# Kernel tuning notes

Hardware: AMD Instinct MI355X
Metric: run time of the kernel (lower is better)

## Reference

```python
import jax, jax.numpy as jnp
import numpy as np
import math

BS, S, D = 1, 2048, 1024
H = 16
DK = D // H  # 64


def _log_sparse_neighbor_mask(seq_len):
    """mask[i,j]=True iff j==i, or j in [i-k, i) with k=seq_len//2, or i-j is a power of 2.
    Matches generate_log_sparse_plus_neighbors_mask(seq_len, seq_len//2)."""
    k = seq_len // 2
    i = jnp.arange(seq_len, dtype=jnp.int32)[:, None]
    j = jnp.arange(seq_len, dtype=jnp.int32)[None, :]
    diff = i - j
    neighbor = (diff >= 0) & (diff <= k)  # includes diagonal (diff==0)
    pow2 = (diff > 0) & ((diff & (diff - 1)) == 0)
    return neighbor | pow2  # [seq_len, seq_len] bool


def setup_inputs() -> dict:
    key = jax.random.key(0)
    ks = jax.random.split(key, 9)
    std = 0.02
    return {
        "Q": jax.random.normal(ks[0], (BS, S, D), dtype=jnp.float32),
        "Wq": jax.random.normal(ks[1], (D, H * DK), dtype=jnp.float32) * std,
        "bq": jnp.zeros((H * DK,), dtype=jnp.float32),
        "Wk": jax.random.normal(ks[2], (D, H * DK), dtype=jnp.float32) * std,
        "bk": jnp.zeros((H * DK,), dtype=jnp.float32),
        "Wv": jax.random.normal(ks[3], (D, H * DK), dtype=jnp.float32) * std,
        "bv": jnp.zeros((H * DK,), dtype=jnp.float32),
        "Wo": jax.random.normal(ks[4], (H * DK, D), dtype=jnp.float32) * std,
        "bo": jnp.zeros((D,), dtype=jnp.float32),
    }


def reference(Q, Wq, bq, Wk, bk, Wv, bv, Wo, bo):
    bs, s, d = Q.shape
    # QKV projections -> [bs, h, s, dk]
    q = (Q @ Wq + bq).reshape(bs, s, H, DK).transpose(0, 2, 1, 3)
    k = (Q @ Wk + bk).reshape(bs, s, H, DK).transpose(0, 2, 1, 3)
    v = (Q @ Wv + bv).reshape(bs, s, H, DK).transpose(0, 2, 1, 3)

    # log_sparse_attention: scale is 1/sqrt(d_k); mask regenerated internally
    mask = _log_sparse_neighbor_mask(s)  # [s, s] bool
    scores = jnp.einsum("bhqd,bhkd->bhqk", q, k) / math.sqrt(DK)
    scores = jnp.where(mask[None, None, :, :], scores, -jnp.inf)
    attn = jax.nn.softmax(scores, axis=-1)  # [bs, h, s, s]
    out = jnp.einsum("bhqk,bhkd->bhqd", attn, v)

    # merge heads + output projection
    out = out.transpose(0, 2, 1, 3).reshape(bs, s, H * DK)
    out = out @ Wo + bo
    return (out, attn)
```

## Files before the change

### kernel.cpp

```cpp
#include <hip/hip_runtime.h>

#define SEQ 2048
#define DM 1024
#define NH 16
#define DKH 64
#define BAND 1024
#define QKV 3072
#define QBLK 32
#define PBW 1064

typedef __attribute__((ext_vector_type(8))) __bf16 bf16x8;
typedef __attribute__((ext_vector_type(4))) __bf16 bf16x4;
typedef __attribute__((ext_vector_type(4))) float f32x4;

static __device__ __forceinline__ f32x4 mfma16(bf16x8 a, bf16x8 b, f32x4 c) {
  return __builtin_amdgcn_mfma_f32_16x16x32_bf16(a, b, c, 0, 0, 0);
}

#define GLOAD16(gp, lp)                                                        \
  __builtin_amdgcn_global_load_lds(                                            \
      (const __attribute__((address_space(1))) void*)(gp),                     \
      (__attribute__((address_space(3))) void*)(lp), 16, 0, 0)

struct PrepArgs {
  const float* win[4];
  __bf16* wout[4];
  const float* Q;
  __bf16* Qb;
};
__global__ void prep(PrepArgs P) {
  int z = blockIdx.z;
  if (z < 4) {
    __shared__ float t[32][33];
    const float* in = P.win[z];
    __bf16* out = P.wout[z];
    int c0 = blockIdx.x * 32, r0 = blockIdx.y * 32;
    int tx = threadIdx.x, ty = threadIdx.y;
    for (int r = ty; r < 32; r += 8)
      t[r][tx] = in[(size_t)(r0 + r) * DM + c0 + tx];
    __syncthreads();
    for (int r = ty; r < 32; r += 8)
      out[(size_t)(c0 + r) * DM + r0 + tx] = (__bf16)t[tx][r];
  } else {
    int t = threadIdx.y * 32 + threadIdx.x;
    int base = (blockIdx.y * 32 + blockIdx.x) * 512 + t;
#pragma unroll
    for (int u = 0; u < 2; u++) {
      int i = base + u * 256;
      float4 v = reinterpret_cast<const float4*>(P.Q)[i];
      bf16x4 o = {(__bf16)v.x, (__bf16)v.y, (__bf16)v.z, (__bf16)v.w};
      reinterpret_cast<bf16x4*>(P.Qb)[i] = o;
    }
  }
}

template <int BM, int BN, bool BF16OUT, bool VOUT>
__global__ __launch_bounds__(256) void gemm_lds(
    const __bf16* __restrict__ A, const __bf16* __restrict__ BT,
    const float* __restrict__ b0, const float* __restrict__ b1,
    const float* __restrict__ b2, float* __restrict__ Cf,
    __bf16* __restrict__ Cb, __bf16* __restrict__ VT, int M, int N, int K) {
  constexpr int BK = 64;
  constexpr int FM = BM / 32;
  constexpr int FN = BN / 32;
  constexpr int LA = BM * BK * 2 / (256 * 16);
  constexpr int LB = BN * BK * 2 / (256 * 16);
  __shared__ __bf16 lA[2][BM * BK];
  __shared__ __bf16 lB[2][BN * BK];
  int tid = threadIdx.x;
  int lane = tid & 63;
  int l15 = lane & 15, lg = lane >> 4;
  int w = tid >> 6;
  int nwg = gridDim.x * gridDim.y;
  int bid = blockIdx.y * gridDim.x + blockIdx.x;
  int swz = (bid & 7) * (nwg >> 3) + (bid >> 3);
  int bx = swz % gridDim.x;
  int by = swz / gridDim.x;
  int row0 = by * BM;
  int col0 = bx * BN;
  int sec = col0 >> 10;
  const float* bias = sec == 0 ? b0 : (sec == 1 ? b1 : b2);
  int cbase = col0 & (DM - 1);
  int wr = (w >> 1) * (BM / 2);
  int wc = (w & 1) * (BN / 2);
  f32x4 acc[FM][FN] = {};

  auto stage = [&](int b, int kt) {
#pragma unroll
    for (int s = 0; s < LA; s++) {
      int u = tid + s * 256;
      int r = u >> 3;
      int cc = (u & 7) ^ (r & 7);
      GLOAD16(A + (size_t)(row0 + r) * K + kt * BK + cc * 8,
              (char*)lA[b] + u * 16);
    }
#pragma unroll
    for (int s = 0; s < LB; s++) {
      int u = tid + s * 256;
      int r = u >> 3;
      int cc = (u & 7) ^ (r & 7);
      GLOAD16(BT + (size_t)(col0 + r) * K + kt * BK + cc * 8,
              (char*)lB[b] + u * 16);
    }
  };

  const int T = K / BK;
  stage(0, 0);
  stage(1, 1);
  for (int t = 0; t < T; t++) {
    if (t + 1 < T)
      asm volatile("s_waitcnt vmcnt(%0)" ::"i"(LA + LB) : "memory");
    else
      asm volatile("s_waitcnt vmcnt(0)" ::: "memory");
    __builtin_amdgcn_s_barrier();
    int cur = t & 1;
    bf16x8 af[2][FM], bfr[2][FN];
#pragma unroll
    for (int kh = 0; kh < 2; kh++) {
#pragma unroll
      for (int mi = 0; mi < FM; mi++) {
        int r = wr + mi * 16 + l15;
        af[kh][mi] = *(const bf16x8*)((const char*)lA[cur] + r * 128 +
                                      ((((kh << 2) | lg) ^ (r & 7)) << 4));
      }
#pragma unroll
      for (int ni = 0; ni < FN; ni++) {
        int r = wc + ni * 16 + l15;
        bfr[kh][ni] = *(const bf16x8*)((const char*)lB[cur] + r * 128 +
                                       ((((kh << 2) | lg) ^ (r & 7)) << 4));
      }
    }
    __builtin_amdgcn_s_setprio(1);
#pragma unroll
    for (int kh = 0; kh < 2; kh++)
#pragma unroll
      for (int mi = 0; mi < FM; mi++)
#pragma unroll
        for (int ni = 0; ni < FN; ni++)
          acc[mi][ni] = mfma16(af[kh][mi], bfr[kh][ni], acc[mi][ni]);
    __builtin_amdgcn_s_setprio(0);
    __builtin_amdgcn_s_barrier();
    if (t + 2 < T) stage(cur, t + 2);
  }

  if (VOUT && sec == 2) {
#pragma unroll
    for (int mi = 0; mi < FM; mi++) {
      int row = row0 + wr + mi * 16 + lg * 4;
#pragma unroll
      for (int ni = 0; ni < FN; ni++) {
        int hd = cbase + wc + ni * 16 + l15;
        float b = bias[hd];
        bf16x4 pk;
#pragma unroll
        for (int r = 0; r < 4; r++) pk[r] = (__bf16)(acc[mi][ni][r] + b);
        *(bf16x4*)&VT[(size_t)hd * SEQ + row] = pk;
      }
    }
    return;
  }
#pragma unroll
  for (int mi = 0; mi < FM; mi++) {
    int row = row0 + wr + mi * 16 + lg * 4;
#pragma unroll
    for (int ni = 0; ni < FN; ni++) {
      int col = col0 + wc + ni * 16 + l15;
      float b = bias[(cbase + wc + ni * 16 + l15) & (DM - 1)];
#pragma unroll
      for (int r = 0; r < 4; r++) {
        float v = acc[mi][ni][r] + b;
        if constexpr (BF16OUT)
          Cb[(size_t)(row + r) * N + col] = (__bf16)v;
        else
          Cf[(size_t)(row + r) * N + col] = v;
      }
    }
  }
}

__global__ __launch_bounds__(256, 2) void attn_fused(
    const __bf16* __restrict__ qkvb, const __bf16* __restrict__ VT,
    float* __restrict__ attn_out, __bf16* __restrict__ pvb) {
  __shared__ __bf16 pbuf[QBLK][PBW];
  __shared__ float wsum[4][QBLK];
  __shared__ float sinv[QBLK];

  int nwg = gridDim.x * gridDim.y;
  int bid = blockIdx.y * gridDim.x + blockIdx.x;
  int swz = (bid & 7) * (nwg >> 3) + (bid >> 3);
  int h = swz / (SEQ / QBLK);
  int i0 = (swz % (SEQ / QBLK)) * QBLK;

  int tid = threadIdx.x, lane = tid & 63, w = tid >> 6;
  int l15 = lane & 15, lg = lane >> 4;

  int jlo = i0 - BAND;
  if (jlo < 0) jlo = 0;
  int ntiles = (i0 + QBLK - jlo) >> 4;
  int n = ntiles * 16;

  const __bf16* qptr0 = qkvb + (size_t)(i0 + l15) * QKV + h * DKH + lg * 8;
  const __bf16* qptr1 = qptr0 + (size_t)16 * QKV;
  bf16x8 aq0 = *(const bf16x8*)qptr0;
  bf16x8 aq1 = *(const bf16x8*)(qptr0 + 32);
  bf16x8 aq2 = *(const bf16x8*)qptr1;
  bf16x8 aq3 = *(const bf16x8*)(qptr1 + 32);
  const __bf16* kbase = qkvb + DM + h * DKH + lg * 8;

  float sm0[4] = {0.f, 0.f, 0.f, 0.f};
  float sm1[4] = {0.f, 0.f, 0.f, 0.f};
  for (int t = w; t < ntiles; t += 4) {
    int jb = jlo + t * 16;
    const __bf16* kptr = kbase + (size_t)(jb + l15) * QKV;
    bf16x8 k0 = *(const bf16x8*)kptr;
    bf16x8 k1 = *(const bf16x8*)(kptr + 32);
    f32x4 acc0 = {0.f, 0.f, 0.f, 0.f};
    f32x4 acc1 = {0.f, 0.f, 0.f, 0.f};
    __builtin_amdgcn_s_setprio(1);
    acc0 = mfma16(aq0, k0, acc0);
    acc0 = mfma16(aq1, k1, acc0);
    acc1 = mfma16(aq2, k0, acc1);
    acc1 = mfma16(aq3, k1, acc1);
    __builtin_amdgcn_s_setprio(0);
    int col = jb + l15;
    int x = jb - jlo + l15;
#pragma unroll
    for (int r = 0; r < 4; r++) {
      int i = i0 + lg * 4 + r;
      float e0 = 0.f;
      if (col <= i && i - col <= BAND) {
        e0 = __expf(acc0[r] * 0.125f);
        sm0[r] += e0;
      }
      pbuf[lg * 4 + r][x] = (__bf16)e0;
      int i2 = i + 16;
      float e1 = 0.f;
      if (col <= i2 && i2 - col <= BAND) {
        e1 = __expf(acc1[r] * 0.125f);
        sm1[r] += e1;
      }
      pbuf[16 + lg * 4 + r][x] = (__bf16)e1;
    }
  }
#pragma unroll
  for (int o = 1; o < 16; o <<= 1)
#pragma unroll
    for (int r = 0; r < 4; r++) {
      sm0[r] += __shfl_xor(sm0[r], o);
      sm1[r] += __shfl_xor(sm1[r], o);
    }
  if (l15 == 0)
#pragma unroll
    for (int r = 0; r < 4; r++) {
      wsum[w][lg * 4 + r] = sm0[r];
      wsum[w][16 + lg * 4 + r] = sm1[r];
    }
  __syncthreads();
  if (tid < QBLK)
    sinv[tid] = 1.f / (wsum[0][tid] + wsum[1][tid] + wsum[2][tid] + wsum[3][tid]);
  __syncthreads();

  f32x4* abase = (f32x4*)(attn_out + ((size_t)h * SEQ + i0) * SEQ);
  for (int idx = tid; idx < QBLK * (SEQ / 4); idx += 256) {
    int row = idx >> 9;
    int j4 = idx & 511;
    int x = j4 * 4 - jlo;
    bool valid = (unsigned)x < (unsigned)n;
    int xc = valid ? x : 0;
    bf16x4 v4 = *(const bf16x4*)&pbuf[row][xc];
    float inv = valid ? sinv[row] : 0.f;
    f32x4 o = {(float)v4[0] * inv, (float)v4[1] * inv, (float)v4[2] * inv,
               (float)v4[3] * inv};
    __builtin_nontemporal_store(o, abase + idx);
  }

  f32x4 acc0 = {0.f, 0.f, 0.f, 0.f};
  f32x4 acc1 = {0.f, 0.f, 0.f, 0.f};
  int d0 = w * 16;
  const __bf16* vtp = VT + ((size_t)h * DKH + d0 + l15) * SEQ;
  for (int kt = 0; kt < ntiles; kt += 2) {
    int kk = kt * 16;
    bf16x8 pa0 = *(const bf16x8*)&pbuf[l15][kk + lg * 8];
    bf16x8 pa1 = *(const bf16x8*)&pbuf[16 + l15][kk + lg * 8];
    bf16x8 vf = *(const bf16x8*)(vtp + jlo + kk + lg * 8);
    __builtin_amdgcn_s_setprio(1);
    acc0 = mfma16(pa0, vf, acc0);
    acc1 = mfma16(pa1, vf, acc1);
    __builtin_amdgcn_s_setprio(0);
  }
#pragma unroll
  for (int r = 0; r < 4; r++) {
    int row = lg * 4 + r;
    pvb[(size_t)(i0 + row) * DM + h * DKH + d0 + l15] =
        (__bf16)(acc0[r] * sinv[row]);
    pvb[(size_t)(i0 + 16 + row) * DM + h * DKH + d0 + l15] =
        (__bf16)(acc1[r] * sinv[16 + row]);
  }
}

extern "C" void kernel_launch(void* const* d_in, const int* in_sizes, int n_in,
                              void* d_out, int out_size, void* d_ws,
                              size_t ws_size, hipStream_t stream) {
  const float* Q = (const float*)d_in[0];
  const float* Wq = (const float*)d_in[1];
  const float* bq = (const float*)d_in[2];
  const float* Wk = (const float*)d_in[3];
  const float* bk = (const float*)d_in[4];
  const float* Wv = (const float*)d_in[5];
  const float* bv = (const float*)d_in[6];
  const float* Wo = (const float*)d_in[7];
  const float* bo = (const float*)d_in[8];
  float* out_proj = (float*)d_out;
  float* attn_out = out_proj + (size_t)SEQ * DM;

  char* ws = (char*)d_ws;
  size_t off = 0;
  auto alloc = [&](size_t bytes) {
    void* p = ws + off;
    off = (off + bytes + 255) & ~(size_t)255;
    return p;
  };
  __bf16* Qb    = (__bf16*)alloc((size_t)SEQ * DM * 2);
  __bf16* WqkvT = (__bf16*)alloc((size_t)QKV * DM * 2);
  __bf16* WoT   = (__bf16*)alloc((size_t)DM * DM * 2);
  __bf16* qkvb  = (__bf16*)alloc((size_t)SEQ * QKV * 2);
  __bf16* VT    = (__bf16*)alloc((size_t)NH * DKH * SEQ * 2);
  __bf16* pvb   = (__bf16*)alloc((size_t)SEQ * DM * 2);

  PrepArgs P;
  P.win[0] = Wq; P.win[1] = Wk; P.win[2] = Wv; P.win[3] = Wo;
  P.wout[0] = WqkvT;
  P.wout[1] = WqkvT + (size_t)DM * DM;
  P.wout[2] = WqkvT + (size_t)2 * DM * DM;
  P.wout[3] = WoT;
  P.Q = Q;
  P.Qb = Qb;
  prep<<<dim3(32, 32, 5), dim3(32, 8), 0, stream>>>(P);

  gemm_lds<64, 128, true, true><<<dim3(QKV / 128, SEQ / 64), 256, 0, stream>>>(
      Qb, WqkvT, bq, bk, bv, nullptr, qkvb, VT, SEQ, QKV, DM);

  attn_fused<<<dim3(SEQ / QBLK, NH), 256, 0, stream>>>(qkvb, VT, attn_out, pvb);

  gemm_lds<64, 64, false, false><<<dim3(DM / 64, SEQ / 64), 256, 0, stream>>>(
      pvb, WoT, bo, bo, bo, out_proj, nullptr, nullptr, SEQ, DM, DM);
}
```

Before: 116.1 us.

## Double attention query block to 64 rows with 512-thread workgroups

Raises the attention query tile from 32 to 64 rows and the workgroup from 256 to 512 threads. Each K tile loaded by a wave now feeds four query row groups instead of two, halving K reloads, and each V fragment is shared across two row groups. The cost is fewer workgroups (512 instead of 1024), a larger LDS buffer of about 140KB, and one workgroup per CU, so there is less latency hiding and worse tail balance. The masked exp work per row is unchanged.

```diff
diff --git a/kernel.cpp b/kernel.cpp
--- a/kernel.cpp
+++ b/kernel.cpp
@@ -6,8 +6,8 @@
 #define DKH 64
 #define BAND 1024
 #define QKV 3072
-#define QBLK 32
-#define PBW 1064
+#define QBLK 64
+#define PBW 1096
 
 typedef __attribute__((ext_vector_type(8))) __bf16 bf16x8;
 typedef __attribute__((ext_vector_type(4))) __bf16 bf16x4;
@@ -178,11 +178,11 @@
   }
 }
 
-__global__ __launch_bounds__(256, 2) void attn_fused(
+__global__ __launch_bounds__(512, 1) void attn_fused(
     const __bf16* __restrict__ qkvb, const __bf16* __restrict__ VT,
     float* __restrict__ attn_out, __bf16* __restrict__ pvb) {
   __shared__ __bf16 pbuf[QBLK][PBW];
-  __shared__ float wsum[4][QBLK];
+  __shared__ float wsum[8][QBLK];
   __shared__ float sinv[QBLK];
 
   int nwg = gridDim.x * gridDim.y;
@@ -199,69 +199,68 @@
   int ntiles = (i0 + QBLK - jlo) >> 4;
   int n = ntiles * 16;
 
-  const __bf16* qptr0 = qkvb + (size_t)(i0 + l15) * QKV + h * DKH + lg * 8;
-  const __bf16* qptr1 = qptr0 + (size_t)16 * QKV;
-  bf16x8 aq0 = *(const bf16x8*)qptr0;
-  bf16x8 aq1 = *(const bf16x8*)(qptr0 + 32);
-  bf16x8 aq2 = *(const bf16x8*)qptr1;
-  bf16x8 aq3 = *(const bf16x8*)(qptr1 + 32);
+  bf16x8 aq[4][2];
+#pragma unroll
+  for (int g = 0; g < 4; g++) {
+    const __bf16* qp =
+        qkvb + (size_t)(i0 + g * 16 + l15) * QKV + h * DKH + lg * 8;
+    aq[g][0] = *(const bf16x8*)qp;
+    aq[g][1] = *(const bf16x8*)(qp + 32);
+  }
   const __bf16* kbase = qkvb + DM + h * DKH + lg * 8;
 
-  float sm0[4] = {0.f, 0.f, 0.f, 0.f};
-  float sm1[4] = {0.f, 0.f, 0.f, 0.f};
-  for (int t = w; t < ntiles; t += 4) {
+  float sm[4][4] = {};
+  for (int t = w; t < ntiles; t += 8) {
     int jb = jlo + t * 16;
     const __bf16* kptr = kbase + (size_t)(jb + l15) * QKV;
     bf16x8 k0 = *(const bf16x8*)kptr;
     bf16x8 k1 = *(const bf16x8*)(kptr + 32);
-    f32x4 acc0 = {0.f, 0.f, 0.f, 0.f};
-    f32x4 acc1 = {0.f, 0.f, 0.f, 0.f};
+    f32x4 acc[4] = {};
     __builtin_amdgcn_s_setprio(1);
-    acc0 = mfma16(aq0, k0, acc0);
-    acc0 = mfma16(aq1, k1, acc0);
-    acc1 = mfma16(aq2, k0, acc1);
-    acc1 = mfma16(aq3, k1, acc1);
+#pragma unroll
+    for (int g = 0; g < 4; g++) {
+      acc[g] = mfma16(aq[g][0], k0, acc[g]);
+      acc[g] = mfma16(aq[g][1], k1, acc[g]);
+    }
     __builtin_amdgcn_s_setprio(0);
     int col = jb + l15;
     int x = jb - jlo + l15;
 #pragma unroll
-    for (int r = 0; r < 4; r++) {
-      int i = i0 + lg * 4 + r;
-      float e0 = 0.f;
-      if (col <= i && i - col <= BAND) {
-        e0 = __expf(acc0[r] * 0.125f);
-        sm0[r] += e0;
-      }
-      pbuf[lg * 4 + r][x] = (__bf16)e0;
-      int i2 = i + 16;
-      float e1 = 0.f;
-      if (col <= i2 && i2 - col <= BAND) {
-        e1 = __expf(acc1[r] * 0.125f);
-        sm1[r] += e1;
-      }
-      pbuf[16 + lg * 4 + r][x] = (__bf16)e1;
+    for (int g = 0; g < 4; g++) {
+#pragma unroll
+      for (int r = 0; r < 4; r++) {
+        int i = i0 + g * 16 + lg * 4 + r;
+        float e = 0.f;
+        if (col <= i && i - col <= BAND) {
+          e = __expf(acc[g][r] * 0.125f);
+          sm[g][r] += e;
+        }
+        pbuf[g * 16 + lg * 4 + r][x] = (__bf16)e;
+      }
     }
   }
 #pragma unroll
   for (int o = 1; o < 16; o <<= 1)
 #pragma unroll
-    for (int r = 0; r < 4; r++) {
-      sm0[r] += __shfl_xor(sm0[r], o);
-      sm1[r] += __shfl_xor(sm1[r], o);
-    }
+    for (int g = 0; g < 4; g++)
+#pragma unroll
+      for (int r = 0; r < 4; r++) sm[g][r] += __shfl_xor(sm[g][r], o);
   if (l15 == 0)
 #pragma unroll
-    for (int r = 0; r < 4; r++) {
-      wsum[w][lg * 4 + r] = sm0[r];
-      wsum[w][16 + lg * 4 + r] = sm1[r];
-    }
+    for (int g = 0; g < 4; g++)
+#pragma unroll
+      for (int r = 0; r < 4; r++) wsum[w][g * 16 + lg * 4 + r] = sm[g][r];
   __syncthreads();
-  if (tid < QBLK)
-    sinv[tid] = 1.f / (wsum[0][tid] + wsum[1][tid] + wsum[2][tid] + wsum[3][tid]);
+  if (tid < QBLK) {
+    float s = 0.f;
+#pragma unroll
+    for (int ww = 0; ww < 8; ww++) s += wsum[ww][tid];
+    sinv[tid] = 1.f / s;
+  }
   __syncthreads();
 
   f32x4* abase = (f32x4*)(attn_out + ((size_t)h * SEQ + i0) * SEQ);
-  for (int idx = tid; idx < QBLK * (SEQ / 4); idx += 256) {
+  for (int idx = tid; idx < QBLK * (SEQ / 4); idx += 512) {
     int row = idx >> 9;
     int j4 = idx & 511;
     int x = j4 * 4 - jlo;
@@ -276,12 +275,13 @@
 
   f32x4 acc0 = {0.f, 0.f, 0.f, 0.f};
   f32x4 acc1 = {0.f, 0.f, 0.f, 0.f};
-  int d0 = w * 16;
+  int g2 = (w >> 2) * 2;
+  int d0 = (w & 3) * 16;
   const __bf16* vtp = VT + ((size_t)h * DKH + d0 + l15) * SEQ;
   for (int kt = 0; kt < ntiles; kt += 2) {
     int kk = kt * 16;
-    bf16x8 pa0 = *(const bf16x8*)&pbuf[l15][kk + lg * 8];
-    bf16x8 pa1 = *(const bf16x8*)&pbuf[16 + l15][kk + lg * 8];
+    bf16x8 pa0 = *(const bf16x8*)&pbuf[g2 * 16 + l15][kk + lg * 8];
+    bf16x8 pa1 = *(const bf16x8*)&pbuf[(g2 + 1) * 16 + l15][kk + lg * 8];
     bf16x8 vf = *(const bf16x8*)(vtp + jlo + kk + lg * 8);
     __builtin_amdgcn_s_setprio(1);
     acc0 = mfma16(pa0, vf, acc0);
@@ -290,11 +290,12 @@
   }
 #pragma unroll
   for (int r = 0; r < 4; r++) {
-    int row = lg * 4 + r;
-    pvb[(size_t)(i0 + row) * DM + h * DKH + d0 + l15] =
-        (__bf16)(acc0[r] * sinv[row]);
-    pvb[(size_t)(i0 + 16 + row) * DM + h * DKH + d0 + l15] =
-        (__bf16)(acc1[r] * sinv[16 + row]);
+    int row0 = g2 * 16 + lg * 4 + r;
+    int row1 = (g2 + 1) * 16 + lg * 4 + r;
+    pvb[(size_t)(i0 + row0) * DM + h * DKH + d0 + l15] =
+        (__bf16)(acc0[r] * sinv[row0]);
+    pvb[(size_t)(i0 + row1) * DM + h * DKH + d0 + l15] =
+        (__bf16)(acc1[r] * sinv[row1]);
   }
 }
 
@@ -340,7 +341,7 @@
   gemm_lds<64, 128, true, true><<<dim3(QKV / 128, SEQ / 64), 256, 0, stream>>>(
       Qb, WqkvT, bq, bk, bv, nullptr, qkvb, VT, SEQ, QKV, DM);
 
-  attn_fused<<<dim3(SEQ / QBLK, NH), 256, 0, stream>>>(qkvb, VT, attn_out, pvb);
+  attn_fused<<<dim3(SEQ / QBLK, NH), 512, 0, stream>>>(qkvb, VT, attn_out, pvb);
 
   gemm_lds<64, 64, false, false><<<dim3(DM / 64, SEQ / 64), 256, 0, stream>>>(
       pvb, WoT, bo, bo, bo, out_proj, nullptr, nullptr, SEQ, DM, DM);
```

Result: slower. 119.0 us (+2.5%).
